# Optimization experiments

Measured on AMD Instinct MI355X. Metric: run time of the kernel, lower is better.

The kernel has to match this reference:

```python
import jax, jax.numpy as jnp
import numpy as np

B = 131072     # batch of observations
OBS = 17       # HalfCheetah-v5 obs dim
ACT = 6        # HalfCheetah-v5 action dim
M = 16         # number of charts / experts
HID = 256      # encoder / value hidden width (hardcoded in module)
GHID = 128     # gate hidden width (hardcoded)
R = 24.0       # chart radius in whitened feature space
BETA = 1.0     # locality prior strength
NEG = -1e9     # masked-logit fill (finite to keep grads clean)
LOG_STD_MIN, LOG_STD_MAX = -20.0, 2.0


def setup_inputs() -> dict:
    key = jax.random.key(0)
    ks = jax.random.split(key, 12)
    def rn(i, shape, sc):
        return jax.random.normal(ks[i], shape, dtype=jnp.float32) * sc
    return {
        "obs": jax.random.normal(ks[0], (B, OBS), dtype=jnp.float32),
        # encoder MLP (only the two hidden tanh layers feed the feature 'feat')
        "W1": rn(1, (OBS, HID), 0.2), "b1": jnp.zeros((HID,), jnp.float32),
        "W2": rn(2, (HID, HID), 0.06), "b2": jnp.zeros((HID,), jnp.float32),
        # gate: Linear(256,128) -> tanh -> Linear(128,m)
        "Wg1": rn(3, (HID, GHID), 0.06), "bg1": jnp.zeros((GHID,), jnp.float32),
        "Wg2": rn(4, (GHID, M), 0.1), "bg2": jnp.zeros((M,), jnp.float32),
        # m local Gaussian heads: mu Linear(256, act), shared log_std param per head
        "muW": rn(5, (M, HID, ACT), 0.06), "mub": jnp.zeros((M, ACT), jnp.float32),
        "log_std": jnp.zeros((M, ACT), jnp.float32),
        # value head: 256 -> 256 -> 256 -> 1 with tanh
        "Wv1": rn(6, (HID, HID), 0.06), "bv1": jnp.zeros((HID,), jnp.float32),
        "Wv2": rn(7, (HID, HID), 0.06), "bv2": jnp.zeros((HID,), jnp.float32),
        "Wv3": rn(8, (HID, 1), 0.06), "bv3": jnp.zeros((1,), jnp.float32),
        # chart cover state (frozen params in the torch module)
        "centers": jax.random.normal(ks[9], (M, HID), dtype=jnp.float32),
        "stats_mean": jnp.zeros((HID,), jnp.float32),
        "stats_var": jnp.ones((HID,), jnp.float32),
    }


def reference(obs, W1, b1, W2, b2, Wg1, bg1, Wg2, bg2, muW, mub, log_std,
              Wv1, bv1, Wv2, bv2, Wv3, bv3, centers, stats_mean, stats_var):
    # shared encoder phi(o): two tanh layers -> feat [B, HID]
    feat = jnp.tanh(jnp.tanh(obs @ W1 + b1) @ W2 + b2)

    # whitened features and squared distances to chart centers (cdist via gram trick)
    zw = (feat - stats_mean) / jnp.sqrt(stats_var + 1e-6)          # [B, HID]
    d2 = jnp.maximum(
        jnp.sum(zw * zw, axis=-1, keepdims=True)
        + jnp.sum(centers * centers, axis=-1)
        - 2.0 * (zw @ centers.T), 0.0)                              # [B, M]
    dists = jnp.sqrt(d2)

    # gate logits + locality prior -beta * ||z - c_i||^2 / r^2
    logits = jnp.tanh(feat @ Wg1 + bg1) @ Wg2 + bg2 - BETA * d2 / (R * R)

    # masked softmax restricted to active charts; nearest chart always active
    active = dists <= R
    nearest = jax.nn.one_hot(jnp.argmin(dists, axis=1), M, dtype=bool)
    active = active | nearest
    g = jax.nn.softmax(jnp.where(active, logits, NEG), axis=1)      # [B, M]

    # local expert heads mu_i(z), then convex combination of mu and log_std
    mus = jnp.einsum('bd,mda->bma', feat, muW) + mub                # [B, M, ACT]
    mu_bar = jnp.einsum('bm,bma->ba', g, mus)                       # [B, ACT]
    s_bar = jnp.clip(g @ log_std, LOG_STD_MIN, LOG_STD_MAX)         # [B, ACT]

    # value head on shared features
    v = (jnp.tanh(jnp.tanh(feat @ Wv1 + bv1) @ Wv2 + bv2) @ Wv3 + bv3)[:, 0]
    return mu_bar, s_bar, v
```

## Files before the change

### kernel.cpp

```cpp
#include <hip/hip_runtime.h>
#include <hip/hip_bf16.h>

#define BDIM 512
#define TB 64
#define OBS_D 17
#define HID 256
#define GHID 128
#define NM 16
#define NACT 6

typedef __attribute__((ext_vector_type(8))) short short8;
typedef __attribute__((ext_vector_type(4))) float f32x4;

#define OFF_W1P    0u
#define OFF_W2P    16384u
#define OFF_WG1P   147456u
#define OFF_WG2P   212992u
#define OFF_CP     217088u
#define OFF_MUWP   225280u
#define OFF_WV1P   274432u
#define OFF_WV2P   405504u
#define OFF_CNORM  536576u
#define OFF_CCONST 536640u

__device__ __forceinline__ float tanh_fast(float x){
  float e = __expf(2.f * x);
  return fmaf(-2.f, __builtin_amdgcn_rcpf(e + 1.f), 1.f);
}
__device__ __forceinline__ short bf16b(float x){
  __hip_bfloat16 h = __float2bfloat16(x);
  return *reinterpret_cast<short*>(&h);
}

__global__ void prep_kernel(const float* __restrict__ W1, const float* __restrict__ W2,
    const float* __restrict__ Wg1, const float* __restrict__ Wg2,
    const float* __restrict__ muW, const float* __restrict__ Wv1, const float* __restrict__ Wv2,
    const float* __restrict__ centers, const float* __restrict__ smean, const float* __restrict__ svar,
    char* __restrict__ ws)
{
  __hip_bfloat16* w1p  = (__hip_bfloat16*)(ws + OFF_W1P);
  __hip_bfloat16* w2p  = (__hip_bfloat16*)(ws + OFF_W2P);
  __hip_bfloat16* wg1p = (__hip_bfloat16*)(ws + OFF_WG1P);
  __hip_bfloat16* wg2p = (__hip_bfloat16*)(ws + OFF_WG2P);
  __hip_bfloat16* cp   = (__hip_bfloat16*)(ws + OFF_CP);
  __hip_bfloat16* muwp = (__hip_bfloat16*)(ws + OFF_MUWP);
  __hip_bfloat16* wv1p = (__hip_bfloat16*)(ws + OFF_WV1P);
  __hip_bfloat16* wv2p = (__hip_bfloat16*)(ws + OFF_WV2P);
  float* cnorm  = (float*)(ws + OFF_CNORM);
  float* cconst = (float*)(ws + OFF_CCONST);

  int gid = blockIdx.x * blockDim.x + threadIdx.x;
  if (gid < NM){
    float s = 0.f; const float* c = centers + gid * HID;
    for (int k = 0; k < HID; ++k) s += c[k] * c[k];
    cnorm[gid] = s;
  } else if (gid < 2*NM){
    int m = gid - NM; float s = 0.f; const float* c = centers + m * HID;
    for (int k = 0; k < HID; ++k) s += smean[k] * rsqrtf(svar[k] + 1e-6f) * c[k];
    cconst[m] = s;
  }

  const int T0 = 8192, T1 = T0+65536, T2 = T1+32768, T3 = T2+2048,
            T4 = T3+4096, T5 = T4+24576, T6 = T5+65536, T7 = T6+65536;
  for (int i = gid; i < T7; i += gridDim.x * blockDim.x){
    float v; __hip_bfloat16* dst;
    if (i < T0){ int idx=i;    int kb8=idx/(256*8); int n=(idx/8)%256; int e=idx&7; int k=kb8*8+e;
      v = (k < OBS_D) ? W1[k*256+n] : 0.f; dst = &w1p[idx]; }
    else if (i < T1){ int idx=i-T0; int kb8=idx/(256*8); int n=(idx/8)%256; int e=idx&7; int k=kb8*8+e;
      v = W2[k*256+n]; dst = &w2p[idx]; }
    else if (i < T2){ int idx=i-T1; int kb8=idx/(128*8); int n=(idx/8)%128; int e=idx&7; int k=kb8*8+e;
      v = Wg1[k*128+n]; dst = &wg1p[idx]; }
    else if (i < T3){ int idx=i-T2; int kb8=idx/(16*8);  int n=(idx/8)%16;  int e=idx&7; int k=kb8*8+e;
      v = Wg2[k*16+n]; dst = &wg2p[idx]; }
    else if (i < T4){ int idx=i-T3; int kb8=idx/(16*8);  int m=(idx/8)%16;  int e=idx&7; int k=kb8*8+e;
      v = centers[m*HID+k] * rsqrtf(svar[k] + 1e-6f); dst = &cp[idx]; }
    else if (i < T5){ int idx=i-T4; int kb8=idx/(96*8);  int n=(idx/8)%96;  int e=idx&7; int k=kb8*8+e;
      int a = n >> 4, m = n & 15;
      v = muW[m*(HID*NACT) + k*NACT + a]; dst = &muwp[idx]; }
    else if (i < T6){ int idx=i-T5; int kb8=idx/(256*8); int n=(idx/8)%256; int e=idx&7; int k=kb8*8+e;
      v = Wv1[k*256+n]; dst = &wv1p[idx]; }
    else            { int idx=i-T6; int kb8=idx/(256*8); int n=(idx/8)%256; int e=idx&7; int k=kb8*8+e;
      v = Wv2[k*256+n]; dst = &wv2p[idx]; }
    *dst = __float2bfloat16(v);
  }
}

__global__ __launch_bounds__(BDIM, 4) void moe_kernel(
  const float* __restrict__ obs,
  const float* __restrict__ b1, const float* __restrict__ b2,
  const float* __restrict__ bg1, const float* __restrict__ bg2,
  const float* __restrict__ mub, const float* __restrict__ lstd,
  const float* __restrict__ bv1, const float* __restrict__ bv2,
  const float* __restrict__ Wv3, const float* __restrict__ bv3,
  const float* __restrict__ smean, const float* __restrict__ svar,
  const char* __restrict__ ws, float* __restrict__ out, int Btot)
{
  const short8* w1p  = (const short8*)(ws + OFF_W1P);
  const short8* w2p  = (const short8*)(ws + OFF_W2P);
  const short8* wg1p = (const short8*)(ws + OFF_WG1P);
  const short8* wg2p = (const short8*)(ws + OFF_WG2P);
  const short8* cp   = (const short8*)(ws + OFF_CP);
  const short8* muwp = (const short8*)(ws + OFF_MUWP);
  const short8* wv1p = (const short8*)(ws + OFF_WV1P);
  const short8* wv2p = (const short8*)(ws + OFF_WV2P);
  const float* cnorm  = (const float*)(ws + OFF_CNORM);
  const float* cconst = (const float*)(ws + OFF_CCONST);

  const int tid = threadIdx.x;
  const int w = tid >> 6, lane = tid & 63, l16 = lane & 15, lk = lane >> 4;
  const int wr = w >> 2, wc = w & 3;
  const int rowg0 = blockIdx.x * TB;
  const int rbase = wr * 32;

  __shared__ __hip_bfloat16 feat_s[32*64*8];
  __shared__ __hip_bfloat16 sc_s[32*64*8];
  __shared__ float part_s[8][64];
  __shared__ float g_s[64*17];

  short8 aO[2];
  #pragma unroll
  for (int rt = 0; rt < 2; ++rt){
    const float* orow = obs + (size_t)(rowg0 + rbase + rt*16 + l16) * OBS_D;
    #pragma unroll
    for (int e = 0; e < 8; ++e){ int k = lk*8 + e; float v = (k < OBS_D) ? orow[k] : 0.f; aO[rt][e] = bf16b(v); }
  }

  #pragma unroll
  for (int ctl = 0; ctl < 4; ++ctl){
    const int ct = wc*4 + ctl;
    short8 B = w1p[lk*256 + ct*16 + l16];
    const int col = ct*16 + l16; const float bb = b1[col];
    #pragma unroll
    for (int rt = 0; rt < 2; ++rt){
      f32x4 acc = {0.f,0.f,0.f,0.f};
      acc = __builtin_amdgcn_mfma_f32_16x16x32_bf16(aO[rt], B, acc, 0,0,0);
      #pragma unroll
      for (int r = 0; r < 4; ++r){
        int row = rbase + rt*16 + lk*4 + r;
        sc_s[((col>>3)*64 + row)*8 + (col&7)] = __float2bfloat16(tanh_fast(acc[r] + bb));
      }
    }
  }
  __syncthreads();

  {
    f32x4 acc2[4][2];
    #pragma unroll
    for (int i = 0; i < 4; ++i)
      #pragma unroll
      for (int j = 0; j < 2; ++j) acc2[i][j] = (f32x4){0.f,0.f,0.f,0.f};
    #pragma unroll
    for (int ck = 0; ck < 8; ++ck){
      short8 A[2];
      #pragma unroll
      for (int rt = 0; rt < 2; ++rt) A[rt] = *(const short8*)&sc_s[((ck*4+lk)*64 + rbase + rt*16 + l16)*8];
      #pragma unroll
      for (int ctl = 0; ctl < 4; ++ctl){
        short8 B = w2p[(ck*4+lk)*256 + (wc*4+ctl)*16 + l16];
        #pragma unroll
        for (int rt = 0; rt < 2; ++rt)
          acc2[ctl][rt] = __builtin_amdgcn_mfma_f32_16x16x32_bf16(A[rt], B, acc2[ctl][rt], 0,0,0);
      }
    }
    float znp[8];
    #pragma unroll
    for (int i = 0; i < 8; ++i) znp[i] = 0.f;
    #pragma unroll
    for (int ctl = 0; ctl < 4; ++ctl){
      const int col = (wc*4+ctl)*16 + l16;
      const float bb = b2[col], mn = smean[col], iv = rsqrtf(svar[col] + 1e-6f);
      #pragma unroll
      for (int rt = 0; rt < 2; ++rt){
        #pragma unroll
        for (int r = 0; r < 4; ++r){
          int row = rbase + rt*16 + lk*4 + r;
          float tf = tanh_fast(acc2[ctl][rt][r] + bb);
          feat_s[((col>>3)*64 + row)*8 + (col&7)] = __float2bfloat16(tf);
          float z = (tf - mn) * iv;
          znp[rt*4+r] += z * z;
        }
      }
    }
    #pragma unroll
    for (int d = 1; d < 16; d <<= 1){
      #pragma unroll
      for (int i = 0; i < 8; ++i) znp[i] += __shfl_xor(znp[i], d, 64);
    }
    if (l16 == 0){
      #pragma unroll
      for (int i = 0; i < 8; ++i) part_s[w][rbase + (i>>2)*16 + lk*4 + (i&3)] = znp[i];
    }
  }
  __syncthreads();

  f32x4 accD = {0.f,0.f,0.f,0.f};
  {
    f32x4 acc3[2][2];
    #pragma unroll
    for (int i = 0; i < 2; ++i)
      #pragma unroll
      for (int j = 0; j < 2; ++j) acc3[i][j] = (f32x4){0.f,0.f,0.f,0.f};
    #pragma unroll
    for (int ck = 0; ck < 8; ++ck){
      short8 A[2];
      #pragma unroll
      for (int rt = 0; rt < 2; ++rt) A[rt] = *(const short8*)&feat_s[((ck*4+lk)*64 + rbase + rt*16 + l16)*8];
      if (wc < 2)
        accD = __builtin_amdgcn_mfma_f32_16x16x32_bf16(A[wc], cp[(ck*4+lk)*16 + l16], accD, 0,0,0);
      #pragma unroll
      for (int ctl = 0; ctl < 2; ++ctl){
        short8 B = wg1p[(ck*4+lk)*128 + (wc*2+ctl)*16 + l16];
        #pragma unroll
        for (int rt = 0; rt < 2; ++rt)
          acc3[ctl][rt] = __builtin_amdgcn_mfma_f32_16x16x32_bf16(A[rt], B, acc3[ctl][rt], 0,0,0);
      }
    }
    #pragma unroll
    for (int ctl = 0; ctl < 2; ++ctl){
      const int col = (wc*2+ctl)*16 + l16;
      const float bb = bg1[col];
      #pragma unroll
      for (int rt = 0; rt < 2; ++rt)
        #pragma unroll
        for (int r = 0; r < 4; ++r){
          int row = rbase + rt*16 + lk*4 + r;
          sc_s[((col>>3)*64 + row)*8 + (col&7)] = __float2bfloat16(tanh_fast(acc3[ctl][rt][r] + bb));
        }
    }
  }
  __syncthreads();

  if (wc < 2){
    const int rw = rbase + wc*16;
    f32x4 accL = {0.f,0.f,0.f,0.f};
    #pragma unroll
    for (int ks = 0; ks < 4; ++ks){
      short8 aT = *(const short8*)&sc_s[((ks*4+lk)*64 + rw + l16)*8];
      accL = __builtin_amdgcn_mfma_f32_16x16x32_bf16(aT, wg2p[(ks*4+lk)*16 + l16], accL, 0,0,0);
    }
    const float cn = cnorm[l16], cc = cconst[l16], bg2v = bg2[l16];
    float gw[4];
    #pragma unroll
    for (int r = 0; r < 4; ++r){
      int rowl = rw + lk*4 + r;
      float znr = part_s[wr*4+0][rowl] + part_s[wr*4+1][rowl]
                + part_s[wr*4+2][rowl] + part_s[wr*4+3][rowl];
      float dot = accD[r] - cc;
      float d2 = fmaxf(znr + cn - 2.f*dot, 0.f);
      float lg = accL[r] + bg2v - d2 * (1.f/576.f);
      float mv = d2; int mi = l16;
      #pragma unroll
      for (int d = 1; d < 16; d <<= 1){
        float ov = __shfl_xor(mv, d, 64); int oi = __shfl_xor(mi, d, 64);
        if (ov < mv || (ov == mv && oi < mi)){ mv = ov; mi = oi; }
      }
      bool act = (d2 <= 576.f) || (mi == l16);
      lg = act ? lg : -1e9f;
      float mx = lg;
      #pragma unroll
      for (int d = 1; d < 16; d <<= 1) mx = fmaxf(mx, __shfl_xor(mx, d, 64));
      float ev = __expf(lg - mx);
      float sm = ev;
      #pragma unroll
      for (int d = 1; d < 16; d <<= 1) sm += __shfl_xor(sm, d, 64);
      gw[r] = ev * __builtin_amdgcn_rcpf(sm);
      g_s[rowl*17 + l16] = gw[r];
    }
    #pragma unroll
    for (int r = 0; r < 4; ++r){
      float sb[6];
      #pragma unroll
      for (int a = 0; a < 6; ++a) sb[a] = gw[r] * lstd[l16*6 + a];
      #pragma unroll
      for (int d = 1; d < 16; d <<= 1){
        #pragma unroll
        for (int a = 0; a < 6; ++a) sb[a] += __shfl_xor(sb[a], d, 64);
      }
      if (l16 == 0){
        int row = rowg0 + rw + lk*4 + r;
        #pragma unroll
        for (int a = 0; a < 6; ++a)
          out[(size_t)6*Btot + (size_t)row*6 + a] = fminf(fmaxf(sb[a], -20.f), 2.f);
      }
    }
  } else {
    f32x4 acc7[4][2];
    #pragma unroll
    for (int i = 0; i < 4; ++i)
      #pragma unroll
      for (int j = 0; j < 2; ++j) acc7[i][j] = (f32x4){0.f,0.f,0.f,0.f};
    #pragma unroll
    for (int ck = 0; ck < 8; ++ck){
      short8 A[2];
      #pragma unroll
      for (int rt = 0; rt < 2; ++rt) A[rt] = *(const short8*)&feat_s[((ck*4+lk)*64 + rbase + rt*16 + l16)*8];
      #pragma unroll
      for (int ctl = 0; ctl < 4; ++ctl){
        short8 B = wv1p[(ck*4+lk)*256 + (8 + (wc-2)*4 + ctl)*16 + l16];
        #pragma unroll
        for (int rt = 0; rt < 2; ++rt)
          acc7[ctl][rt] = __builtin_amdgcn_mfma_f32_16x16x32_bf16(A[rt], B, acc7[ctl][rt], 0,0,0);
      }
    }
    #pragma unroll
    for (int ctl = 0; ctl < 4; ++ctl){
      const int col = (8 + (wc-2)*4 + ctl)*16 + l16;
      const float bb = bv1[col];
      #pragma unroll
      for (int rt = 0; rt < 2; ++rt)
        #pragma unroll
        for (int r = 0; r < 4; ++r){
          int row = rbase + rt*16 + lk*4 + r;
          sc_s[((col>>3)*64 + row)*8 + (col&7)] = __float2bfloat16(tanh_fast(acc7[ctl][rt][r] + bb));
        }
    }
  }
  __syncthreads();

  if (wc < 2){
    f32x4 acc7[4][2];
    #pragma unroll
    for (int i = 0; i < 4; ++i)
      #pragma unroll
      for (int j = 0; j < 2; ++j) acc7[i][j] = (f32x4){0.f,0.f,0.f,0.f};
    #pragma unroll
    for (int ck = 0; ck < 8; ++ck){
      short8 A[2];
      #pragma unroll
      for (int rt = 0; rt < 2; ++rt) A[rt] = *(const short8*)&feat_s[((ck*4+lk)*64 + rbase + rt*16 + l16)*8];
      #pragma unroll
      for (int ctl = 0; ctl < 4; ++ctl){
        short8 B = wv1p[(ck*4+lk)*256 + (wc*4 + ctl)*16 + l16];
        #pragma unroll
        for (int rt = 0; rt < 2; ++rt)
          acc7[ctl][rt] = __builtin_amdgcn_mfma_f32_16x16x32_bf16(A[rt], B, acc7[ctl][rt], 0,0,0);
      }
    }
    #pragma unroll
    for (int ctl = 0; ctl < 4; ++ctl){
      const int col = (wc*4 + ctl)*16 + l16;
      const float bb = bv1[col];
      #pragma unroll
      for (int rt = 0; rt < 2; ++rt)
        #pragma unroll
        for (int r = 0; r < 4; ++r){
          int row = rbase + rt*16 + lk*4 + r;
          sc_s[((col>>3)*64 + row)*8 + (col&7)] = __float2bfloat16(tanh_fast(acc7[ctl][rt][r] + bb));
        }
    }
  } else {
    f32x4 accM[3][2];
    #pragma unroll
    for (int i = 0; i < 3; ++i)
      #pragma unroll
      for (int j = 0; j < 2; ++j) accM[i][j] = (f32x4){0.f,0.f,0.f,0.f};
    #pragma unroll
    for (int ck = 0; ck < 8; ++ck){
      short8 A[2];
      #pragma unroll
      for (int rt = 0; rt < 2; ++rt) A[rt] = *(const short8*)&feat_s[((ck*4+lk)*64 + rbase + rt*16 + l16)*8];
      #pragma unroll
      for (int al = 0; al < 3; ++al){
        short8 B = muwp[(ck*4+lk)*96 + ((wc-2)*3 + al)*16 + l16];
        #pragma unroll
        for (int rt = 0; rt < 2; ++rt)
          accM[al][rt] = __builtin_amdgcn_mfma_f32_16x16x32_bf16(A[rt], B, accM[al][rt], 0,0,0);
      }
    }
    #pragma unroll
    for (int al = 0; al < 3; ++al){
      const int a = (wc-2)*3 + al;
      const float mubv = mub[l16*6 + a];
      #pragma unroll
      for (int rt = 0; rt < 2; ++rt){
        #pragma unroll
        for (int r = 0; r < 4; ++r){
          int row = rbase + rt*16 + lk*4 + r;
          float m = (accM[al][rt][r] + mubv) * g_s[row*17 + l16];
          #pragma unroll
          for (int d = 1; d < 16; d <<= 1) m += __shfl_xor(m, d, 64);
          if (l16 == 0) out[(size_t)(rowg0 + row)*6 + a] = m;
        }
      }
    }
  }
  __syncthreads();

  {
    f32x4 acc8[4][2];
    #pragma unroll
    for (int i = 0; i < 4; ++i)
      #pragma unroll
      for (int j = 0; j < 2; ++j) acc8[i][j] = (f32x4){0.f,0.f,0.f,0.f};
    #pragma unroll
    for (int ck = 0; ck < 8; ++ck){
      short8 A[2];
      #pragma unroll
      for (int rt = 0; rt < 2; ++rt) A[rt] = *(const short8*)&sc_s[((ck*4+lk)*64 + rbase + rt*16 + l16)*8];
      #pragma unroll
      for (int ctl = 0; ctl < 4; ++ctl){
        short8 B = wv2p[(ck*4+lk)*256 + (wc*4+ctl)*16 + l16];
        #pragma unroll
        for (int rt = 0; rt < 2; ++rt)
          acc8[ctl][rt] = __builtin_amdgcn_mfma_f32_16x16x32_bf16(A[rt], B, acc8[ctl][rt], 0,0,0);
      }
    }
    float vpp[8];
    #pragma unroll
    for (int i = 0; i < 8; ++i) vpp[i] = 0.f;
    #pragma unroll
    for (int ctl = 0; ctl < 4; ++ctl){
      const int col = (wc*4+ctl)*16 + l16;
      const float bb = bv2[col], w3 = Wv3[col];
      #pragma unroll
      for (int rt = 0; rt < 2; ++rt)
        #pragma unroll
        for (int r = 0; r < 4; ++r)
          vpp[rt*4+r] += tanh_fast(acc8[ctl][rt][r] + bb) * w3;
    }
    #pragma unroll
    for (int d = 1; d < 16; d <<= 1){
      #pragma unroll
      for (int i = 0; i < 8; ++i) vpp[i] += __shfl_xor(vpp[i], d, 64);
    }
    if (l16 == 0){
      #pragma unroll
      for (int i = 0; i < 8; ++i) part_s[w][rbase + (i>>2)*16 + lk*4 + (i&3)] = vpp[i];
    }
  }
  __syncthreads();
  if (tid < 64){
    int g = tid >> 5;
    float v = part_s[g*4+0][tid] + part_s[g*4+1][tid]
            + part_s[g*4+2][tid] + part_s[g*4+3][tid] + bv3[0];
    out[(size_t)12*Btot + rowg0 + tid] = v;
  }
}

extern "C" void kernel_launch(void* const* d_in, const int* in_sizes, int n_in,
                              void* d_out, int out_size, void* d_ws, size_t ws_size,
                              hipStream_t stream){
  const float* obs = (const float*)d_in[0];
  const float* W1  = (const float*)d_in[1];  const float* b1  = (const float*)d_in[2];
  const float* W2  = (const float*)d_in[3];  const float* b2  = (const float*)d_in[4];
  const float* Wg1 = (const float*)d_in[5];  const float* bg1 = (const float*)d_in[6];
  const float* Wg2 = (const float*)d_in[7];  const float* bg2 = (const float*)d_in[8];
  const float* muW = (const float*)d_in[9];  const float* mub = (const float*)d_in[10];
  const float* lstd= (const float*)d_in[11];
  const float* Wv1 = (const float*)d_in[12]; const float* bv1 = (const float*)d_in[13];
  const float* Wv2 = (const float*)d_in[14]; const float* bv2 = (const float*)d_in[15];
  const float* Wv3 = (const float*)d_in[16]; const float* bv3 = (const float*)d_in[17];
  const float* centers = (const float*)d_in[18];
  const float* smean   = (const float*)d_in[19];
  const float* svar    = (const float*)d_in[20];
  int Btot = in_sizes[0] / OBS_D;
  char* ws = (char*)d_ws;

  hipLaunchKernelGGL(prep_kernel, dim3(512), dim3(256), 0, stream,
      W1, W2, Wg1, Wg2, muW, Wv1, Wv2, centers, smean, svar, ws);
  hipLaunchKernelGGL(moe_kernel, dim3(Btot / TB), dim3(BDIM), 0, stream,
      obs, b1, b2, bg1, bg2, mub, lstd, bv1, bv2, Wv3, bv3, smean, svar,
      (const char*)ws, (float*)d_out, Btot);
}
```

Measured before the change: 185.4 us.

## Split fused MoE kernel into encoder kernel and role-split heads kernel

Replaces the single fused per-tile kernel with two kernels. The first computes the encoder features, writes them to global workspace in bf16 and stores the whitened squared norms. The second launches twice as many blocks, one role doing the value head and the other doing gate, softmax and expert mixing. This aims to balance work across waves and raise occupancy, since the old kernel left half its waves idle in several stages. The cost is a round trip of the feature matrix through global memory (about 64 MB) plus one extra launch, and it needs a large workspace, with a fallback to the fused kernel when the workspace is too small.

```diff
diff --git a/kernel.cpp b/kernel.cpp
--- a/kernel.cpp
+++ b/kernel.cpp
@@ -22,6 +22,8 @@
 #define OFF_WV2P   405504u
 #define OFF_CNORM  536576u
 #define OFF_CCONST 536640u
+#define OFF_ZN     540672u
+#define OFF_FEATG  1064960u
 
 __device__ __forceinline__ float tanh_fast(float x){
   float e = __expf(2.f * x);
@@ -85,6 +87,355 @@
   }
 }
 
+__global__ __launch_bounds__(BDIM, 8) void feat_kernel(
+  const float* __restrict__ obs,
+  const float* __restrict__ b1, const float* __restrict__ b2,
+  const float* __restrict__ smean, const float* __restrict__ svar,
+  char* __restrict__ ws, int Btot)
+{
+  const short8* w1p = (const short8*)(ws + OFF_W1P);
+  const short8* w2p = (const short8*)(ws + OFF_W2P);
+  __hip_bfloat16* featg = (__hip_bfloat16*)(ws + OFF_FEATG);
+  float* zn_g = (float*)(ws + OFF_ZN);
+
+  const int tid = threadIdx.x;
+  const int w = tid >> 6, lane = tid & 63, l16 = lane & 15, lk = lane >> 4;
+  const int wr = w >> 2, wc = w & 3;
+  const int rowg0 = blockIdx.x * TB;
+  const int rbase = wr * 32;
+
+  __shared__ __hip_bfloat16 sc_s[32*64*8];
+  __shared__ float part_s[8][64];
+
+  short8 aO[2];
+  #pragma unroll
+  for (int rt = 0; rt < 2; ++rt){
+    const float* orow = obs + (size_t)(rowg0 + rbase + rt*16 + l16) * OBS_D;
+    #pragma unroll
+    for (int e = 0; e < 8; ++e){ int k = lk*8 + e; float v = (k < OBS_D) ? orow[k] : 0.f; aO[rt][e] = bf16b(v); }
+  }
+
+  #pragma unroll
+  for (int ctl = 0; ctl < 4; ++ctl){
+    const int ct = wc*4 + ctl;
+    short8 B = w1p[lk*256 + ct*16 + l16];
+    const int col = ct*16 + l16; const float bb = b1[col];
+    #pragma unroll
+    for (int rt = 0; rt < 2; ++rt){
+      f32x4 acc = {0.f,0.f,0.f,0.f};
+      acc = __builtin_amdgcn_mfma_f32_16x16x32_bf16(aO[rt], B, acc, 0,0,0);
+      #pragma unroll
+      for (int r = 0; r < 4; ++r){
+        int row = rbase + rt*16 + lk*4 + r;
+        sc_s[((col>>3)*64 + row)*8 + (col&7)] = __float2bfloat16(tanh_fast(acc[r] + bb));
+      }
+    }
+  }
+  __syncthreads();
+
+  {
+    f32x4 acc2[4][2];
+    #pragma unroll
+    for (int i = 0; i < 4; ++i)
+      #pragma unroll
+      for (int j = 0; j < 2; ++j) acc2[i][j] = (f32x4){0.f,0.f,0.f,0.f};
+    #pragma unroll
+    for (int ck = 0; ck < 8; ++ck){
+      short8 A[2];
+      #pragma unroll
+      for (int rt = 0; rt < 2; ++rt) A[rt] = *(const short8*)&sc_s[((ck*4+lk)*64 + rbase + rt*16 + l16)*8];
+      #pragma unroll
+      for (int ctl = 0; ctl < 4; ++ctl){
+        short8 B = w2p[(ck*4+lk)*256 + (wc*4+ctl)*16 + l16];
+        #pragma unroll
+        for (int rt = 0; rt < 2; ++rt)
+          acc2[ctl][rt] = __builtin_amdgcn_mfma_f32_16x16x32_bf16(A[rt], B, acc2[ctl][rt], 0,0,0);
+      }
+    }
+    float znp[8];
+    #pragma unroll
+    for (int i = 0; i < 8; ++i) znp[i] = 0.f;
+    #pragma unroll
+    for (int ctl = 0; ctl < 4; ++ctl){
+      const int col = (wc*4+ctl)*16 + l16;
+      const int c = col >> 3, e = col & 7;
+      const float bb = b2[col], mn = smean[col], iv = rsqrtf(svar[col] + 1e-6f);
+      #pragma unroll
+      for (int rt = 0; rt < 2; ++rt){
+        #pragma unroll
+        for (int r = 0; r < 4; ++r){
+          int rowl = rbase + rt*16 + lk*4 + r;
+          float tf = tanh_fast(acc2[ctl][rt][r] + bb);
+          featg[((size_t)c*Btot + rowg0 + rowl)*8 + e] = __float2bfloat16(tf);
+          float z = (tf - mn) * iv;
+          znp[rt*4+r] += z * z;
+        }
+      }
+    }
+    #pragma unroll
+    for (int d = 1; d < 16; d <<= 1){
+      #pragma unroll
+      for (int i = 0; i < 8; ++i) znp[i] += __shfl_xor(znp[i], d, 64);
+    }
+    if (l16 == 0){
+      #pragma unroll
+      for (int i = 0; i < 8; ++i) part_s[w][rbase + (i>>2)*16 + lk*4 + (i&3)] = znp[i];
+    }
+  }
+  __syncthreads();
+  if (tid < 64){
+    int g = tid >> 5;
+    zn_g[rowg0 + tid] = part_s[g*4+0][tid] + part_s[g*4+1][tid]
+                      + part_s[g*4+2][tid] + part_s[g*4+3][tid];
+  }
+}
+
+__global__ __launch_bounds__(BDIM, 6) void heads_kernel(
+  const float* __restrict__ bg1, const float* __restrict__ bg2,
+  const float* __restrict__ mub, const float* __restrict__ lstd,
+  const float* __restrict__ bv1, const float* __restrict__ bv2,
+  const float* __restrict__ Wv3, const float* __restrict__ bv3,
+  const char* __restrict__ ws, float* __restrict__ out, int Btot)
+{
+  const short8* wg1p = (const short8*)(ws + OFF_WG1P);
+  const short8* wg2p = (const short8*)(ws + OFF_WG2P);
+  const short8* cp   = (const short8*)(ws + OFF_CP);
+  const short8* muwp = (const short8*)(ws + OFF_MUWP);
+  const short8* wv1p = (const short8*)(ws + OFF_WV1P);
+  const short8* wv2p = (const short8*)(ws + OFF_WV2P);
+  const float* cnorm  = (const float*)(ws + OFF_CNORM);
+  const float* cconst = (const float*)(ws + OFF_CCONST);
+  const __hip_bfloat16* featg = (const __hip_bfloat16*)(ws + OFF_FEATG);
+  const float* zn_g = (const float*)(ws + OFF_ZN);
+
+  const int tid = threadIdx.x;
+  const int w = tid >> 6, lane = tid & 63, l16 = lane & 15, lk = lane >> 4;
+  const int wr = w >> 2, wc = w & 3;
+  const int role = blockIdx.x & 1;
+  const int rowg0 = (blockIdx.x >> 1) * TB;
+  const int rbase = wr * 32;
+
+  __shared__ __hip_bfloat16 sc_s[32*64*8];
+  __shared__ float part_s[8][64];
+  __shared__ float g_s[64*17];
+
+  if (role == 0){
+    {
+      f32x4 acc7[4][2];
+      #pragma unroll
+      for (int i = 0; i < 4; ++i)
+        #pragma unroll
+        for (int j = 0; j < 2; ++j) acc7[i][j] = (f32x4){0.f,0.f,0.f,0.f};
+      #pragma unroll
+      for (int ck = 0; ck < 8; ++ck){
+        short8 A[2];
+        #pragma unroll
+        for (int rt = 0; rt < 2; ++rt)
+          A[rt] = *(const short8*)&featg[((size_t)(ck*4+lk)*Btot + rowg0 + rbase + rt*16 + l16)*8];
+        #pragma unroll
+        for (int ctl = 0; ctl < 4; ++ctl){
+          short8 B = wv1p[(ck*4+lk)*256 + (wc*4+ctl)*16 + l16];
+          #pragma unroll
+          for (int rt = 0; rt < 2; ++rt)
+            acc7[ctl][rt] = __builtin_amdgcn_mfma_f32_16x16x32_bf16(A[rt], B, acc7[ctl][rt], 0,0,0);
+        }
+      }
+      #pragma unroll
+      for (int ctl = 0; ctl < 4; ++ctl){
+        const int col = (wc*4+ctl)*16 + l16;
+        const float bb = bv1[col];
+        #pragma unroll
+        for (int rt = 0; rt < 2; ++rt)
+          #pragma unroll
+          for (int r = 0; r < 4; ++r){
+            int row = rbase + rt*16 + lk*4 + r;
+            sc_s[((col>>3)*64 + row)*8 + (col&7)] = __float2bfloat16(tanh_fast(acc7[ctl][rt][r] + bb));
+          }
+      }
+    }
+    __syncthreads();
+    {
+      f32x4 acc8[4][2];
+      #pragma unroll
+      for (int i = 0; i < 4; ++i)
+        #pragma unroll
+        for (int j = 0; j < 2; ++j) acc8[i][j] = (f32x4){0.f,0.f,0.f,0.f};
+      #pragma unroll
+      for (int ck = 0; ck < 8; ++ck){
+        short8 A[2];
+        #pragma unroll
+        for (int rt = 0; rt < 2; ++rt) A[rt] = *(const short8*)&sc_s[((ck*4+lk)*64 + rbase + rt*16 + l16)*8];
+        #pragma unroll
+        for (int ctl = 0; ctl < 4; ++ctl){
+          short8 B = wv2p[(ck*4+lk)*256 + (wc*4+ctl)*16 + l16];
+          #pragma unroll
+          for (int rt = 0; rt < 2; ++rt)
+            acc8[ctl][rt] = __builtin_amdgcn_mfma_f32_16x16x32_bf16(A[rt], B, acc8[ctl][rt], 0,0,0);
+        }
+      }
+      float vpp[8];
+      #pragma unroll
+      for (int i = 0; i < 8; ++i) vpp[i] = 0.f;
+      #pragma unroll
+      for (int ctl = 0; ctl < 4; ++ctl){
+        const int col = (wc*4+ctl)*16 + l16;
+        const float bb = bv2[col], w3 = Wv3[col];
+        #pragma unroll
+        for (int rt = 0; rt < 2; ++rt)
+          #pragma unroll
+          for (int r = 0; r < 4; ++r)
+            vpp[rt*4+r] += tanh_fast(acc8[ctl][rt][r] + bb) * w3;
+      }
+      #pragma unroll
+      for (int d = 1; d < 16; d <<= 1){
+        #pragma unroll
+        for (int i = 0; i < 8; ++i) vpp[i] += __shfl_xor(vpp[i], d, 64);
+      }
+      if (l16 == 0){
+        #pragma unroll
+        for (int i = 0; i < 8; ++i) part_s[w][rbase + (i>>2)*16 + lk*4 + (i&3)] = vpp[i];
+      }
+    }
+    __syncthreads();
+    if (tid < 64){
+      int g = tid >> 5;
+      float v = part_s[g*4+0][tid] + part_s[g*4+1][tid]
+              + part_s[g*4+2][tid] + part_s[g*4+3][tid] + bv3[0];
+      out[(size_t)12*Btot + rowg0 + tid] = v;
+    }
+  } else {
+    f32x4 accD = {0.f,0.f,0.f,0.f};
+    {
+      f32x4 acc3[2][2];
+      #pragma unroll
+      for (int i = 0; i < 2; ++i)
+        #pragma unroll
+        for (int j = 0; j < 2; ++j) acc3[i][j] = (f32x4){0.f,0.f,0.f,0.f};
+      #pragma unroll
+      for (int ck = 0; ck < 8; ++ck){
+        short8 A[2];
+        #pragma unroll
+        for (int rt = 0; rt < 2; ++rt)
+          A[rt] = *(const short8*)&featg[((size_t)(ck*4+lk)*Btot + rowg0 + rbase + rt*16 + l16)*8];
+        if (wc < 2)
+          accD = __builtin_amdgcn_mfma_f32_16x16x32_bf16(A[wc], cp[(ck*4+lk)*16 + l16], accD, 0,0,0);
+        #pragma unroll
+        for (int ctl = 0; ctl < 2; ++ctl){
+          short8 B = wg1p[(ck*4+lk)*128 + (wc*2+ctl)*16 + l16];
+          #pragma unroll
+          for (int rt = 0; rt < 2; ++rt)
+            acc3[ctl][rt] = __builtin_amdgcn_mfma_f32_16x16x32_bf16(A[rt], B, acc3[ctl][rt], 0,0,0);
+        }
+      }
+      #pragma unroll
+      for (int ctl = 0; ctl < 2; ++ctl){
+        const int col = (wc*2+ctl)*16 + l16;
+        const float bb = bg1[col];
+        #pragma unroll
+        for (int rt = 0; rt < 2; ++rt)
+          #pragma unroll
+          for (int r = 0; r < 4; ++r){
+            int row = rbase + rt*16 + lk*4 + r;
+            sc_s[((col>>3)*64 + row)*8 + (col&7)] = __float2bfloat16(tanh_fast(acc3[ctl][rt][r] + bb));
+          }
+      }
+    }
+    __syncthreads();
+    if (wc < 2){
+      const int rw = rbase + wc*16;
+      f32x4 accL = {0.f,0.f,0.f,0.f};
+      #pragma unroll
+      for (int ks = 0; ks < 4; ++ks){
+        short8 aT = *(const short8*)&sc_s[((ks*4+lk)*64 + rw + l16)*8];
+        accL = __builtin_amdgcn_mfma_f32_16x16x32_bf16(aT, wg2p[(ks*4+lk)*16 + l16], accL, 0,0,0);
+      }
+      const float cn = cnorm[l16], cc = cconst[l16], bg2v = bg2[l16];
+      float gw[4];
+      #pragma unroll
+      for (int r = 0; r < 4; ++r){
+        int rowl = rw + lk*4 + r;
+        float znr = zn_g[rowg0 + rowl];
+        float dot = accD[r] - cc;
+        float d2 = fmaxf(znr + cn - 2.f*dot, 0.f);
+        float lg = accL[r] + bg2v - d2 * (1.f/576.f);
+        float mv = d2; int mi = l16;
+        #pragma unroll
+        for (int d = 1; d < 16; d <<= 1){
+          float ov = __shfl_xor(mv, d, 64); int oi = __shfl_xor(mi, d, 64);
+          if (ov < mv || (ov == mv && oi < mi)){ mv = ov; mi = oi; }
+        }
+        bool act = (d2 <= 576.f) || (mi == l16);
+        lg = act ? lg : -1e9f;
+        float mx = lg;
+        #pragma unroll
+        for (int d = 1; d < 16; d <<= 1) mx = fmaxf(mx, __shfl_xor(mx, d, 64));
+        float ev = __expf(lg - mx);
+        float sm = ev;
+        #pragma unroll
+        for (int d = 1; d < 16; d <<= 1) sm += __shfl_xor(sm, d, 64);
+        gw[r] = ev * __builtin_amdgcn_rcpf(sm);
+        g_s[rowl*17 + l16] = gw[r];
+      }
+      #pragma unroll
+      for (int r = 0; r < 4; ++r){
+        float sb[6];
+        #pragma unroll
+        for (int a = 0; a < 6; ++a) sb[a] = gw[r] * lstd[l16*6 + a];
+        #pragma unroll
+        for (int d = 1; d < 16; d <<= 1){
+          #pragma unroll
+          for (int a = 0; a < 6; ++a) sb[a] += __shfl_xor(sb[a], d, 64);
+        }
+        if (l16 == 0){
+          int row = rowg0 + rw + lk*4 + r;
+          #pragma unroll
+          for (int a = 0; a < 6; ++a)
+            out[(size_t)6*Btot + (size_t)row*6 + a] = fminf(fmaxf(sb[a], -20.f), 2.f);
+        }
+      }
+    }
+    __syncthreads();
+    if (wc < 3){
+      const int a0 = wc*2;
+      f32x4 accM[2][2];
+      #pragma unroll
+      for (int i = 0; i < 2; ++i)
+        #pragma unroll
+        for (int j = 0; j < 2; ++j) accM[i][j] = (f32x4){0.f,0.f,0.f,0.f};
+      #pragma unroll
+      for (int ck = 0; ck < 8; ++ck){
+        short8 A[2];
+        #pragma unroll
+        for (int rt = 0; rt < 2; ++rt)
+          A[rt] = *(const short8*)&featg[((size_t)(ck*4+lk)*Btot + rowg0 + rbase + rt*16 + l16)*8];
+        #pragma unroll
+        for (int al = 0; al < 2; ++al){
+          short8 B = muwp[(ck*4+lk)*96 + (a0+al)*16 + l16];
+          #pragma unroll
+          for (int rt = 0; rt < 2; ++rt)
+            accM[al][rt] = __builtin_amdgcn_mfma_f32_16x16x32_bf16(A[rt], B, accM[al][rt], 0,0,0);
+        }
+      }
+      #pragma unroll
+      for (int al = 0; al < 2; ++al){
+        const int a = a0 + al;
+        const float mubv = mub[l16*6 + a];
+        #pragma unroll
+        for (int rt = 0; rt < 2; ++rt){
+          #pragma unroll
+          for (int r = 0; r < 4; ++r){
+            int row = rbase + rt*16 + lk*4 + r;
+            float m = (accM[al][rt][r] + mubv) * g_s[row*17 + l16];
+            #pragma unroll
+            for (int d = 1; d < 16; d <<= 1) m += __shfl_xor(m, d, 64);
+            if (l16 == 0) out[(size_t)(rowg0 + row)*6 + a] = m;
+          }
+        }
+      }
+    }
+  }
+}
+
 __global__ __launch_bounds__(BDIM, 4) void moe_kernel(
   const float* __restrict__ obs,
   const float* __restrict__ b1, const float* __restrict__ b2,
@@ -124,7 +475,6 @@
     #pragma unroll
     for (int e = 0; e < 8; ++e){ int k = lk*8 + e; float v = (k < OBS_D) ? orow[k] : 0.f; aO[rt][e] = bf16b(v); }
   }
-
   #pragma unroll
   for (int ctl = 0; ctl < 4; ++ctl){
     const int ct = wc*4 + ctl;
@@ -142,7 +492,6 @@
     }
   }
   __syncthreads();
-
   {
     f32x4 acc2[4][2];
     #pragma unroll
@@ -192,7 +541,6 @@
     }
   }
   __syncthreads();
-
   f32x4 accD = {0.f,0.f,0.f,0.f};
   {
     f32x4 acc3[2][2];
@@ -229,7 +577,6 @@
     }
   }
   __syncthreads();
-
   if (wc < 2){
     const int rw = rbase + wc*16;
     f32x4 accL = {0.f,0.f,0.f,0.f};
@@ -316,7 +663,6 @@
     }
   }
   __syncthreads();
-
   if (wc < 2){
     f32x4 acc7[4][2];
     #pragma unroll
@@ -385,7 +731,6 @@
     }
   }
   __syncthreads();
-
   {
     f32x4 acc8[4][2];
     #pragma unroll
@@ -458,7 +803,16 @@
 
   hipLaunchKernelGGL(prep_kernel, dim3(512), dim3(256), 0, stream,
       W1, W2, Wg1, Wg2, muW, Wv1, Wv2, centers, smean, svar, ws);
-  hipLaunchKernelGGL(moe_kernel, dim3(Btot / TB), dim3(BDIM), 0, stream,
-      obs, b1, b2, bg1, bg2, mub, lstd, bv1, bv2, Wv3, bv3, smean, svar,
-      (const char*)ws, (float*)d_out, Btot);
+
+  size_t need = (size_t)OFF_FEATG + (size_t)Btot * 512u;
+  if (ws_size >= need){
+    hipLaunchKernelGGL(feat_kernel, dim3(Btot / TB), dim3(BDIM), 0, stream,
+        obs, b1, b2, smean, svar, ws, Btot);
+    hipLaunchKernelGGL(heads_kernel, dim3((Btot / TB) * 2), dim3(BDIM), 0, stream,
+        bg1, bg2, mub, lstd, bv1, bv2, Wv3, bv3, (const char*)ws, (float*)d_out, Btot);
+  } else {
+    hipLaunchKernelGGL(moe_kernel, dim3(Btot / TB), dim3(BDIM), 0, stream,
+        obs, b1, b2, bg1, bg2, mub, lstd, bv1, bv2, Wv3, bv3, smean, svar,
+        (const char*)ws, (float*)d_out, Btot);
+  }
 }
```

New measurement: 258.4 us. +39.4%, slower.

## Keep gate weights in registers for mu head, fold biases into MFMA accumulators

Applied to the files above, without the earlier changes.

The gating waves (wc<2) now compute the mixture-of-experts mu projection themselves, so the softmax weights stay in registers and the g_s shared-memory staging array is removed. The value-layer-1 work is reassigned so the other waves cover both halves of that layer across the two phases. Biases are folded into the initial MFMA accumulator values instead of being added after, and tanh uses exp2 with a prescaled constant. This reduces LDS traffic and per-element adds, but it shifts the work balance between wave groups and changes the per-wave MFMA mix.

```diff
diff --git a/kernel.cpp b/kernel.cpp
--- a/kernel.cpp
+++ b/kernel.cpp
@@ -24,7 +24,7 @@
 #define OFF_CCONST 536640u
 
 __device__ __forceinline__ float tanh_fast(float x){
-  float e = __expf(2.f * x);
+  float e = __builtin_amdgcn_exp2f(x * 2.8853900817779268f);
   return fmaf(-2.f, __builtin_amdgcn_rcpf(e + 1.f), 1.f);
 }
 __device__ __forceinline__ short bf16b(float x){
@@ -115,7 +115,6 @@
   __shared__ __hip_bfloat16 feat_s[32*64*8];
   __shared__ __hip_bfloat16 sc_s[32*64*8];
   __shared__ float part_s[8][64];
-  __shared__ float g_s[64*17];
 
   short8 aO[2];
   #pragma unroll
@@ -132,12 +131,12 @@
     const int col = ct*16 + l16; const float bb = b1[col];
     #pragma unroll
     for (int rt = 0; rt < 2; ++rt){
-      f32x4 acc = {0.f,0.f,0.f,0.f};
+      f32x4 acc = {bb, bb, bb, bb};
       acc = __builtin_amdgcn_mfma_f32_16x16x32_bf16(aO[rt], B, acc, 0,0,0);
       #pragma unroll
       for (int r = 0; r < 4; ++r){
         int row = rbase + rt*16 + lk*4 + r;
-        sc_s[((col>>3)*64 + row)*8 + (col&7)] = __float2bfloat16(tanh_fast(acc[r] + bb));
+        sc_s[((col>>3)*64 + row)*8 + (col&7)] = __float2bfloat16(tanh_fast(acc[r]));
       }
     }
   }
@@ -146,9 +145,11 @@
   {
     f32x4 acc2[4][2];
     #pragma unroll
-    for (int i = 0; i < 4; ++i)
-      #pragma unroll
-      for (int j = 0; j < 2; ++j) acc2[i][j] = (f32x4){0.f,0.f,0.f,0.f};
+    for (int ctl = 0; ctl < 4; ++ctl){
+      const float bb = b2[(wc*4+ctl)*16 + l16];
+      #pragma unroll
+      for (int j = 0; j < 2; ++j) acc2[ctl][j] = (f32x4){bb, bb, bb, bb};
+    }
     #pragma unroll
     for (int ck = 0; ck < 8; ++ck){
       short8 A[2];
@@ -168,13 +169,13 @@
     #pragma unroll
     for (int ctl = 0; ctl < 4; ++ctl){
       const int col = (wc*4+ctl)*16 + l16;
-      const float bb = b2[col], mn = smean[col], iv = rsqrtf(svar[col] + 1e-6f);
+      const float mn = smean[col], iv = rsqrtf(svar[col] + 1e-6f);
       #pragma unroll
       for (int rt = 0; rt < 2; ++rt){
         #pragma unroll
         for (int r = 0; r < 4; ++r){
           int row = rbase + rt*16 + lk*4 + r;
-          float tf = tanh_fast(acc2[ctl][rt][r] + bb);
+          float tf = tanh_fast(acc2[ctl][rt][r]);
           feat_s[((col>>3)*64 + row)*8 + (col&7)] = __float2bfloat16(tf);
           float z = (tf - mn) * iv;
           znp[rt*4+r] += z * z;
@@ -197,9 +198,11 @@
   {
     f32x4 acc3[2][2];
     #pragma unroll
-    for (int i = 0; i < 2; ++i)
-      #pragma unroll
-      for (int j = 0; j < 2; ++j) acc3[i][j] = (f32x4){0.f,0.f,0.f,0.f};
+    for (int ctl = 0; ctl < 2; ++ctl){
+      const float bb = bg1[(wc*2+ctl)*16 + l16];
+      #pragma unroll
+      for (int j = 0; j < 2; ++j) acc3[ctl][j] = (f32x4){bb, bb, bb, bb};
+    }
     #pragma unroll
     for (int ck = 0; ck < 8; ++ck){
       short8 A[2];
@@ -218,28 +221,28 @@
     #pragma unroll
     for (int ctl = 0; ctl < 2; ++ctl){
       const int col = (wc*2+ctl)*16 + l16;
-      const float bb = bg1[col];
       #pragma unroll
       for (int rt = 0; rt < 2; ++rt)
         #pragma unroll
         for (int r = 0; r < 4; ++r){
           int row = rbase + rt*16 + lk*4 + r;
-          sc_s[((col>>3)*64 + row)*8 + (col&7)] = __float2bfloat16(tanh_fast(acc3[ctl][rt][r] + bb));
+          sc_s[((col>>3)*64 + row)*8 + (col&7)] = __float2bfloat16(tanh_fast(acc3[ctl][rt][r]));
         }
     }
   }
   __syncthreads();
 
+  float gw[4];
+  const int rw = rbase + (wc & 1)*16;
   if (wc < 2){
-    const int rw = rbase + wc*16;
-    f32x4 accL = {0.f,0.f,0.f,0.f};
+    const float bg2v = bg2[l16];
+    f32x4 accL = {bg2v, bg2v, bg2v, bg2v};
     #pragma unroll
     for (int ks = 0; ks < 4; ++ks){
       short8 aT = *(const short8*)&sc_s[((ks*4+lk)*64 + rw + l16)*8];
       accL = __builtin_amdgcn_mfma_f32_16x16x32_bf16(aT, wg2p[(ks*4+lk)*16 + l16], accL, 0,0,0);
     }
-    const float cn = cnorm[l16], cc = cconst[l16], bg2v = bg2[l16];
-    float gw[4];
+    const float cn = cnorm[l16], cc = cconst[l16];
     #pragma unroll
     for (int r = 0; r < 4; ++r){
       int rowl = rw + lk*4 + r;
@@ -247,7 +250,7 @@
                 + part_s[wr*4+2][rowl] + part_s[wr*4+3][rowl];
       float dot = accD[r] - cc;
       float d2 = fmaxf(znr + cn - 2.f*dot, 0.f);
-      float lg = accL[r] + bg2v - d2 * (1.f/576.f);
+      float lg = accL[r] - d2 * (1.f/576.f);
       float mv = d2; int mi = l16;
       #pragma unroll
       for (int d = 1; d < 16; d <<= 1){
@@ -264,7 +267,6 @@
       #pragma unroll
       for (int d = 1; d < 16; d <<= 1) sm += __shfl_xor(sm, d, 64);
       gw[r] = ev * __builtin_amdgcn_rcpf(sm);
-      g_s[rowl*17 + l16] = gw[r];
     }
     #pragma unroll
     for (int r = 0; r < 4; ++r){
@@ -286,9 +288,11 @@
   } else {
     f32x4 acc7[4][2];
     #pragma unroll
-    for (int i = 0; i < 4; ++i)
-      #pragma unroll
-      for (int j = 0; j < 2; ++j) acc7[i][j] = (f32x4){0.f,0.f,0.f,0.f};
+    for (int ctl = 0; ctl < 4; ++ctl){
+      const float bb = bv1[(8 + (wc-2)*4 + ctl)*16 + l16];
+      #pragma unroll
+      for (int j = 0; j < 2; ++j) acc7[ctl][j] = (f32x4){bb, bb, bb, bb};
+    }
     #pragma unroll
     for (int ck = 0; ck < 8; ++ck){
       short8 A[2];
@@ -305,24 +309,51 @@
     #pragma unroll
     for (int ctl = 0; ctl < 4; ++ctl){
       const int col = (8 + (wc-2)*4 + ctl)*16 + l16;
-      const float bb = bv1[col];
       #pragma unroll
       for (int rt = 0; rt < 2; ++rt)
         #pragma unroll
         for (int r = 0; r < 4; ++r){
           int row = rbase + rt*16 + lk*4 + r;
-          sc_s[((col>>3)*64 + row)*8 + (col&7)] = __float2bfloat16(tanh_fast(acc7[ctl][rt][r] + bb));
+          sc_s[((col>>3)*64 + row)*8 + (col&7)] = __float2bfloat16(tanh_fast(acc7[ctl][rt][r]));
         }
     }
   }
   __syncthreads();
 
   if (wc < 2){
+    f32x4 accM[6];
+    #pragma unroll
+    for (int al = 0; al < 6; ++al){
+      const float mb = mub[l16*6 + al];
+      accM[al] = (f32x4){mb, mb, mb, mb};
+    }
+    #pragma unroll
+    for (int ck = 0; ck < 8; ++ck){
+      short8 A = *(const short8*)&feat_s[((ck*4+lk)*64 + rw + l16)*8];
+      #pragma unroll
+      for (int al = 0; al < 6; ++al){
+        short8 B = muwp[(ck*4+lk)*96 + al*16 + l16];
+        accM[al] = __builtin_amdgcn_mfma_f32_16x16x32_bf16(A, B, accM[al], 0,0,0);
+      }
+    }
+    #pragma unroll
+    for (int al = 0; al < 6; ++al){
+      #pragma unroll
+      for (int r = 0; r < 4; ++r){
+        float m = accM[al][r] * gw[r];
+        #pragma unroll
+        for (int d = 1; d < 16; d <<= 1) m += __shfl_xor(m, d, 64);
+        if (l16 == 0) out[(size_t)(rowg0 + rw + lk*4 + r)*6 + al] = m;
+      }
+    }
+  } else {
     f32x4 acc7[4][2];
     #pragma unroll
-    for (int i = 0; i < 4; ++i)
-      #pragma unroll
-      for (int j = 0; j < 2; ++j) acc7[i][j] = (f32x4){0.f,0.f,0.f,0.f};
+    for (int ctl = 0; ctl < 4; ++ctl){
+      const float bb = bv1[((wc-2)*4 + ctl)*16 + l16];
+      #pragma unroll
+      for (int j = 0; j < 2; ++j) acc7[ctl][j] = (f32x4){bb, bb, bb, bb};
+    }
     #pragma unroll
     for (int ck = 0; ck < 8; ++ck){
       short8 A[2];
@@ -330,7 +361,7 @@
       for (int rt = 0; rt < 2; ++rt) A[rt] = *(const short8*)&feat_s[((ck*4+lk)*64 + rbase + rt*16 + l16)*8];
       #pragma unroll
       for (int ctl = 0; ctl < 4; ++ctl){
-        short8 B = wv1p[(ck*4+lk)*256 + (wc*4 + ctl)*16 + l16];
+        short8 B = wv1p[(ck*4+lk)*256 + ((wc-2)*4 + ctl)*16 + l16];
         #pragma unroll
         for (int rt = 0; rt < 2; ++rt)
           acc7[ctl][rt] = __builtin_amdgcn_mfma_f32_16x16x32_bf16(A[rt], B, acc7[ctl][rt], 0,0,0);
@@ -338,50 +369,14 @@
     }
     #pragma unroll
     for (int ctl = 0; ctl < 4; ++ctl){
-      const int col = (wc*4 + ctl)*16 + l16;
-      const float bb = bv1[col];
+      const int col = ((wc-2)*4 + ctl)*16 + l16;
       #pragma unroll
       for (int rt = 0; rt < 2; ++rt)
         #pragma unroll
         for (int r = 0; r < 4; ++r){
           int row = rbase + rt*16 + lk*4 + r;
-          sc_s[((col>>3)*64 + row)*8 + (col&7)] = __float2bfloat16(tanh_fast(acc7[ctl][rt][r] + bb));
+          sc_s[((col>>3)*64 + row)*8 + (col&7)] = __float2bfloat16(tanh_fast(acc7[ctl][rt][r]));
         }
-    }
-  } else {
-    f32x4 accM[3][2];
-    #pragma unroll
-    for (int i = 0; i < 3; ++i)
-      #pragma unroll
-      for (int j = 0; j < 2; ++j) accM[i][j] = (f32x4){0.f,0.f,0.f,0.f};
-    #pragma unroll
-    for (int ck = 0; ck < 8; ++ck){
-      short8 A[2];
-      #pragma unroll
-      for (int rt = 0; rt < 2; ++rt) A[rt] = *(const short8*)&feat_s[((ck*4+lk)*64 + rbase + rt*16 + l16)*8];
-      #pragma unroll
-      for (int al = 0; al < 3; ++al){
-        short8 B = muwp[(ck*4+lk)*96 + ((wc-2)*3 + al)*16 + l16];
-        #pragma unroll
-        for (int rt = 0; rt < 2; ++rt)
-          accM[al][rt] = __builtin_amdgcn_mfma_f32_16x16x32_bf16(A[rt], B, accM[al][rt], 0,0,0);
-      }
-    }
-    #pragma unroll
-    for (int al = 0; al < 3; ++al){
-      const int a = (wc-2)*3 + al;
-      const float mubv = mub[l16*6 + a];
-      #pragma unroll
-      for (int rt = 0; rt < 2; ++rt){
-        #pragma unroll
-        for (int r = 0; r < 4; ++r){
-          int row = rbase + rt*16 + lk*4 + r;
-          float m = (accM[al][rt][r] + mubv) * g_s[row*17 + l16];
-          #pragma unroll
-          for (int d = 1; d < 16; d <<= 1) m += __shfl_xor(m, d, 64);
-          if (l16 == 0) out[(size_t)(rowg0 + row)*6 + a] = m;
-        }
-      }
     }
   }
   __syncthreads();
@@ -389,9 +384,11 @@
   {
     f32x4 acc8[4][2];
     #pragma unroll
-    for (int i = 0; i < 4; ++i)
-      #pragma unroll
-      for (int j = 0; j < 2; ++j) acc8[i][j] = (f32x4){0.f,0.f,0.f,0.f};
+    for (int ctl = 0; ctl < 4; ++ctl){
+      const float bb = bv2[(wc*4+ctl)*16 + l16];
+      #pragma unroll
+      for (int j = 0; j < 2; ++j) acc8[ctl][j] = (f32x4){bb, bb, bb, bb};
+    }
     #pragma unroll
     for (int ck = 0; ck < 8; ++ck){
       short8 A[2];
@@ -410,13 +407,12 @@
     for (int i = 0; i < 8; ++i) vpp[i] = 0.f;
     #pragma unroll
     for (int ctl = 0; ctl < 4; ++ctl){
-      const int col = (wc*4+ctl)*16 + l16;
-      const float bb = bv2[col], w3 = Wv3[col];
+      const float w3 = Wv3[(wc*4+ctl)*16 + l16];
       #pragma unroll
       for (int rt = 0; rt < 2; ++rt)
         #pragma unroll
         for (int r = 0; r < 4; ++r)
-          vpp[rt*4+r] += tanh_fast(acc8[ctl][rt][r] + bb) * w3;
+          vpp[rt*4+r] += tanh_fast(acc8[ctl][rt][r]) * w3;
     }
     #pragma unroll
     for (int d = 1; d < 16; d <<= 1){
```

After: 185.3 us. Within noise of the previous version (-0.0%).
